# Performance work log

Measured on AMD Instinct MI355X. Metric: run time of the kernel, lower is better.

Reference implementation:

```python
import jax, jax.numpy as jnp
import numpy as np

VOCAB, EMBED, HID, LAYERS, NGRAPH = 50000, 128, 256, 3, 128

def setup_inputs() -> dict:
    key = jax.random.key(0)
    ks = jax.random.split(key, 16)
    N, E = 50000, 800000
    x_lex = jax.random.randint(ks[0], (N,), 0, VOCAB)
    edge_index = jax.random.randint(ks[1], (2, E), 0, N)
    batch = jnp.sort(jax.random.randint(ks[2], (N,), 0, NGRAPH))
    s = lambda k, shp, fan: jax.random.normal(k, shp, jnp.float32) * (1.0 / np.sqrt(fan))
    return {
        "x_lex": x_lex, "edge_index": edge_index, "batch": batch,
        "embed_table": s(ks[3], (VOCAB, EMBED), EMBED),
        "W_proj": s(ks[4], (HID, EMBED), EMBED),                 # F.linear random-projection branch
        "ggnn_weight": s(ks[5], (LAYERS, HID, HID), HID),        # per-layer message transform
        "W_ih": s(ks[6], (3 * HID, HID), HID), "b_ih": jnp.zeros((3 * HID,), jnp.float32),
        "W_hh": s(ks[7], (3 * HID, HID), HID), "b_hh": jnp.zeros((3 * HID,), jnp.float32),
        "W1": s(ks[8], (HID // 4, HID), HID), "b1": jnp.zeros((HID // 4,), jnp.float32),
        "W2": s(ks[9], (1, HID // 4), HID // 4), "b2": jnp.zeros((1,), jnp.float32),
    }

def _gru_cell(a, h, W_ih, b_ih, W_hh, b_hh):
    gi = a @ W_ih.T + b_ih   # [N, 3H]
    gh = h @ W_hh.T + b_hh
    i_r, i_z, i_n = jnp.split(gi, 3, axis=-1)
    h_r, h_z, h_n = jnp.split(gh, 3, axis=-1)
    r = jax.nn.sigmoid(i_r + h_r)
    z = jax.nn.sigmoid(i_z + h_z)
    n = jnp.tanh(i_n + r * h_n)
    return (1.0 - z) * n + z * h

def reference(x_lex, edge_index, batch, embed_table, W_proj, ggnn_weight,
              W_ih, b_ih, W_hh, b_hh, W1, b1, W2, b2):
    N = x_lex.shape[0]
    x = embed_table[x_lex]                 # [N, EMBED]
    x = x @ W_proj.T                       # project to HID (embed_dim != hidden_dim branch)
    src, dst = edge_index[0], edge_index[1]
    h = x
    for i in range(LAYERS):
        m = h @ ggnn_weight[i]             # [N, HID] per-layer linear
        agg = jax.ops.segment_sum(m[src], dst, num_segments=N)  # scatter-add aggregation
        h = _gru_cell(agg, h, W_ih, b_ih, W_hh, b_hh)
    h_pool = jax.ops.segment_max(h, batch, num_segments=NGRAPH)  # global_max_pool [G, HID]
    logits = jax.nn.relu(h_pool @ W1.T + b1) @ W2.T + b2          # [G, 1]
    return (logits, h_pool)
```

## Files before the change

kernel.cpp:

```cpp
#include <hip/hip_runtime.h>
#include <math.h>

constexpr int HID = 256;

typedef __attribute__((ext_vector_type(8))) short bf16x8;
typedef __attribute__((ext_vector_type(4))) float f32x4;

__device__ __forceinline__ float bf2f(unsigned short u){
    union { unsigned int i; float f; } v; v.i = ((unsigned int)u) << 16; return v.f;
}
__device__ __forceinline__ unsigned short f2bf(float f){
    union { float f; unsigned int i; } v; v.f = f;
    return (unsigned short)((v.i + 0x7fffu + ((v.i >> 16) & 1u)) >> 16);
}
__device__ __forceinline__ float sigm(float x){ return 1.f / (1.f + __expf(-x)); }

__device__ __forceinline__ int xcd_chunk(int bid, int nwg){
    int q = nwg >> 3, r = nwg & 7;
    int xcd = bid & 7, pos = bid >> 3;
    return (xcd < r) ? xcd * (q + 1) + pos : r * (q + 1) + (xcd - r) * q + pos;
}

__device__ __forceinline__ void gll16(const unsigned short* g, unsigned short* l){
    __builtin_amdgcn_global_load_lds(
        (const __attribute__((address_space(1))) void*)g,
        (__attribute__((address_space(3))) void*)l, 16, 0, 0);
}

__global__ void k_prep(const float* __restrict__ Wproj, const float* __restrict__ Wih,
                       const float* __restrict__ Whh, const float* __restrict__ Wg,
                       const float* __restrict__ embed, const int* __restrict__ idx,
                       unsigned short* __restrict__ wproj, unsigned short* __restrict__ wih,
                       unsigned short* __restrict__ whh, unsigned short* __restrict__ wg,
                       unsigned short* __restrict__ x0, int Nn, int EMB){
    const long n1 = (long)HID * EMB, n2 = 3L * HID * HID;
    const long n5 = (long)Nn * EMB;
    const long tot = n1 + 3 * n2 + n5;
    for (long i = blockIdx.x * (long)blockDim.x + threadIdx.x; i < tot;
         i += (long)gridDim.x * blockDim.x){
        long j = i;
        if (j < n1){ wproj[j] = f2bf(Wproj[j]); continue; }
        j -= n1;
        if (j < n2){ wih[j] = f2bf(Wih[j]); continue; }
        j -= n2;
        if (j < n2){ whh[j] = f2bf(Whh[j]); continue; }
        j -= n2;
        if (j < n2){ wg[j] = f2bf(Wg[j]); continue; }
        j -= n2;
        int row = (int)(j / EMB), k = (int)(j % EMB);
        x0[j] = f2bf(embed[(size_t)idx[row] * EMB + k]);
    }
}

__global__ void k_deg(const int* __restrict__ dst, int E, int* __restrict__ deg){
    int i = blockIdx.x*blockDim.x + threadIdx.x;
    if (i < E) atomicAdd(&deg[dst[i]], 1);
}

__global__ void k_scanA(const int* __restrict__ deg, int N, int* __restrict__ bsum){
    __shared__ int red[512];
    int b = blockIdx.x, tid = threadIdx.x;
    int i = b * 512 + tid;
    red[tid] = (i < N) ? deg[i] : 0;
    __syncthreads();
    for (int o = 256; o > 0; o >>= 1){
        if (tid < o) red[tid] += red[tid + o];
        __syncthreads();
    }
    if (tid == 0) bsum[b] = red[0];
}

__global__ void k_scanB(int* __restrict__ bsum, int nb){
    __shared__ int s[1024];
    int tid = threadIdx.x;
    s[tid] = (tid < nb) ? bsum[tid] : 0;
    __syncthreads();
    for (int o = 1; o < 1024; o <<= 1){
        int v = (tid >= o) ? s[tid - o] : 0;
        __syncthreads();
        s[tid] += v;
        __syncthreads();
    }
    if (tid < nb) bsum[tid] = (tid > 0) ? s[tid - 1] : 0;
    if (tid == nb) bsum[nb] = s[nb - 1];
}

__global__ void k_scanC(const int* __restrict__ deg, int N, const int* __restrict__ bsum,
                        int* __restrict__ off){
    __shared__ int s[512];
    int b = blockIdx.x, tid = threadIdx.x;
    int i = b * 512 + tid;
    int v = (i < N) ? deg[i] : 0;
    s[tid] = v;
    __syncthreads();
    for (int o = 1; o < 512; o <<= 1){
        int t = (tid >= o) ? s[tid - o] : 0;
        __syncthreads();
        s[tid] += t;
        __syncthreads();
    }
    int ex = bsum[b] + ((tid > 0) ? s[tid - 1] : 0);
    if (i < N) off[i] = ex;
    else if (i == N) off[N] = ex;
}

__global__ void k_fill(const int* __restrict__ src, const int* __restrict__ dst, int E,
                       const int* __restrict__ off, int* __restrict__ cursor,
                       int* __restrict__ csr_src){
    int i = blockIdx.x*blockDim.x + threadIdx.x;
    if (i < E){
        int d = dst[i];
        int p = off[d] + atomicAdd(&cursor[d], 1);
        csr_src[p] = src[i];
    }
}

__global__ void k_agg(const unsigned short* __restrict__ h, const int* __restrict__ off,
                      const int* __restrict__ csr, unsigned short* __restrict__ out, int N){
    int wave = threadIdx.x >> 6, lane = threadIdx.x & 63;
    int d = blockIdx.x * 8 + wave * 2 + (lane >> 5);
    if (d >= N) return;
    int c = (lane & 31) * 8;
    float a[8] = {};
    int s0 = off[d], s1 = off[d + 1];
    int j = s0;
    for (; j + 3 < s1; j += 4){
        int sA = csr[j], sB = csr[j + 1], sC = csr[j + 2], sD = csr[j + 3];
        bf16x8 vA = *(const bf16x8*)(h + (size_t)sA * HID + c);
        bf16x8 vB = *(const bf16x8*)(h + (size_t)sB * HID + c);
        bf16x8 vC = *(const bf16x8*)(h + (size_t)sC * HID + c);
        bf16x8 vD = *(const bf16x8*)(h + (size_t)sD * HID + c);
        #pragma unroll
        for (int q = 0; q < 8; q++)
            a[q] += (bf2f((unsigned short)vA[q]) + bf2f((unsigned short)vB[q]))
                  + (bf2f((unsigned short)vC[q]) + bf2f((unsigned short)vD[q]));
    }
    for (; j < s1; j++){
        bf16x8 vA = *(const bf16x8*)(h + (size_t)csr[j] * HID + c);
        #pragma unroll
        for (int q = 0; q < 8; q++) a[q] += bf2f((unsigned short)vA[q]);
    }
    bf16x8 o;
    #pragma unroll
    for (int q = 0; q < 8; q++) o[q] = (short)f2bf(a[q]);
    *(bf16x8*)(out + (size_t)d * HID + c) = o;
}

__global__ __launch_bounds__(256, 3) void k_mmS(
    const unsigned short* __restrict__ A, const unsigned short* __restrict__ B,
    unsigned short* __restrict__ C, int M, int N, int K,
    int nbx, long lsB, long lsC)
{
    __shared__ __align__(16) unsigned short sm[3 * 1024 * 8];
    const int tid = threadIdx.x, w = tid >> 6, l = tid & 63;
    const int wm = w >> 1, wn = w & 1, lr = l & 15, lk = l >> 4;

    const int orig = xcd_chunk(blockIdx.x, gridDim.x);
    const int layer = orig / nbx, sub = orig % nbx;
    B += layer * lsB;
    C += layer * lsC;
    const int nby = N >> 7;
    const long row0 = (long)(sub / nby) * 128;
    const int  col0 = (sub % nby) * 128;

    long aoff0, aoff1, boff0, boff1;
    {
        int r0 = tid >> 2,          kc0 = tid & 3;
        int r1 = (tid + 256) >> 2,  kc1 = tid & 3;
        long g0 = row0 + r0; if (g0 > M - 1) g0 = M - 1;
        long g1 = row0 + r1; if (g1 > M - 1) g1 = M - 1;
        aoff0 = g0 * (long)K + (kc0 ^ ((r0 >> 1) & 3)) * 8;
        aoff1 = g1 * (long)K + (kc1 ^ ((r1 >> 1) & 3)) * 8;
        boff0 = (long)(col0 + r0) * K + (kc0 ^ ((r0 >> 1) & 3)) * 8;
        boff1 = (long)(col0 + r1) * K + (kc1 ^ ((r1 >> 1) & 3)) * 8;
    }
    auto STAGE = [&](int T, int buf){
        const int ka = T * 32;
        unsigned short* d = sm + (size_t)buf * 8192;
        gll16(A + aoff0 + ka, d + (0 * 256 + w * 64) * 8);
        gll16(A + aoff1 + ka, d + (1 * 256 + w * 64) * 8);
        gll16(B + boff0 + ka, d + (2 * 256 + w * 64) * 8);
        gll16(B + boff1 + ka, d + (3 * 256 + w * 64) * 8);
    };

    int raddrA[4], raddrB[4];
    #pragma unroll
    for (int i = 0; i < 4; i++){
        int ra = wm * 64 + i * 16 + lr;
        raddrA[i] = (ra * 4 + (lk ^ ((ra >> 1) & 3))) * 8;
        int rb = wn * 64 + i * 16 + lr;
        raddrB[i] = (512 + rb * 4 + (lk ^ ((rb >> 1) & 3))) * 8;
    }

    const int NT = K >> 5;
    STAGE(0, 0);
    STAGE(1, 1);

    f32x4 acc[4][4] = {};
    for (int t = 0; t < NT; t++){
        if (t < NT - 1) asm volatile("s_waitcnt vmcnt(4)" ::: "memory");
        else            asm volatile("s_waitcnt vmcnt(0)" ::: "memory");
        __builtin_amdgcn_s_barrier();
        if (t + 2 < NT) STAGE(t + 2, (t + 2) % 3);

        const unsigned short* bufp = sm + (size_t)(t % 3) * 8192;
        bf16x8 af[4], bfb[4];
        #pragma unroll
        for (int i = 0; i < 4; i++){
            af[i]  = *(const bf16x8*)(bufp + raddrA[i]);
            bfb[i] = *(const bf16x8*)(bufp + raddrB[i]);
        }
        __builtin_amdgcn_s_setprio(1);
        #pragma unroll
        for (int mi = 0; mi < 4; mi++)
            #pragma unroll
            for (int ni = 0; ni < 4; ni++)
                acc[mi][ni] = __builtin_amdgcn_mfma_f32_16x16x32_bf16(af[mi], bfb[ni], acc[mi][ni], 0, 0, 0);
        __builtin_amdgcn_s_setprio(0);
    }

    #pragma unroll
    for (int mi = 0; mi < 4; mi++)
        #pragma unroll
        for (int ni = 0; ni < 4; ni++)
            #pragma unroll
            for (int r = 0; r < 4; r++){
                long row = row0 + wm * 64 + mi * 16 + lk * 4 + r;
                if (row < M){
                    int col = col0 + wn * 64 + ni * 16 + lr;
                    C[row * (long)N + col] = f2bf(acc[mi][ni][r]);
                }
            }
}

__global__ __launch_bounds__(256, 2) void k_gru(
    const unsigned short* __restrict__ AGG, const unsigned short* __restrict__ H,
    const unsigned short* __restrict__ WE, const unsigned short* __restrict__ WH,
    const float* __restrict__ bih, const float* __restrict__ bhh,
    unsigned short* __restrict__ HN, int M)
{
    __shared__ __align__(16) unsigned short sm[3 * 1280 * 8];
    const int tid = threadIdx.x, w = tid >> 6, l = tid & 63;
    const int wm = w >> 1, wn = w & 1, lr = l & 15, lk = l >> 4;
    const int orig = xcd_chunk(blockIdx.x, gridDim.x);
    const long row0 = (long)(orig >> 2) * 128;
    const int  c0 = (orig & 3) * 64;

    long aoff0, aoff1, boff0, boff1, boff2;
    {
        int r0 = tid >> 2,         kc = tid & 3;
        int r1 = (tid + 256) >> 2;
        long g0 = row0 + r0; if (g0 > M - 1) g0 = M - 1;
        long g1 = row0 + r1; if (g1 > M - 1) g1 = M - 1;
        aoff0 = g0 * HID + (kc ^ ((r0 >> 1) & 3)) * 8;
        aoff1 = g1 * HID + (kc ^ ((r1 >> 1) & 3)) * 8;
        int rr = tid >> 2;
        long sw = (kc ^ ((rr >> 1) & 3)) * 8;
        boff0 = (long)(0 * HID + c0 + rr) * HID + sw;
        boff1 = (long)(1 * HID + c0 + rr) * HID + sw;
        boff2 = (long)(2 * HID + c0 + rr) * HID + sw;
    }
    auto STAGE = [&](int T, int buf){
        const unsigned short* As = (T < 8) ? AGG : H;
        const unsigned short* Bs = (T < 8) ? WE  : WH;
        const int ka = (T & 7) * 32;
        unsigned short* d = sm + (size_t)buf * 10240;
        gll16(As + aoff0 + ka, d + (0 * 256 + w * 64) * 8);
        gll16(As + aoff1 + ka, d + (1 * 256 + w * 64) * 8);
        gll16(Bs + boff0 + ka, d + (2 * 256 + w * 64) * 8);
        gll16(Bs + boff1 + ka, d + (3 * 256 + w * 64) * 8);
        gll16(Bs + boff2 + ka, d + (4 * 256 + w * 64) * 8);
    };

    int raddrA[4], raddrB[3][2];
    #pragma unroll
    for (int i = 0; i < 4; i++){
        int ra = wm * 64 + i * 16 + lr;
        raddrA[i] = (ra * 4 + (lk ^ ((ra >> 1) & 3))) * 8;
    }
    #pragma unroll
    for (int j = 0; j < 3; j++)
        #pragma unroll
        for (int ni = 0; ni < 2; ni++){
            int rb = wn * 32 + ni * 16 + lr;
            raddrB[j][ni] = (512 + j * 256 + rb * 4 + (lk ^ ((rb >> 1) & 3))) * 8;
        }

    f32x4 aR[4][2] = {}, aZ[4][2] = {}, aI[4][2] = {}, aHn[4][2] = {};

    auto STEP = [&](const unsigned short* bufp, f32x4 (&aX)[4][2]){
        bf16x8 a[4], bb[3][2];
        #pragma unroll
        for (int i = 0; i < 4; i++) a[i] = *(const bf16x8*)(bufp + raddrA[i]);
        #pragma unroll
        for (int j = 0; j < 3; j++)
            #pragma unroll
            for (int ni = 0; ni < 2; ni++)
                bb[j][ni] = *(const bf16x8*)(bufp + raddrB[j][ni]);
        __builtin_amdgcn_s_setprio(1);
        #pragma unroll
        for (int ni = 0; ni < 2; ni++)
            #pragma unroll
            for (int mi = 0; mi < 4; mi++){
                aR[mi][ni] = __builtin_amdgcn_mfma_f32_16x16x32_bf16(a[mi], bb[0][ni], aR[mi][ni], 0, 0, 0);
                aZ[mi][ni] = __builtin_amdgcn_mfma_f32_16x16x32_bf16(a[mi], bb[1][ni], aZ[mi][ni], 0, 0, 0);
                aX[mi][ni] = __builtin_amdgcn_mfma_f32_16x16x32_bf16(a[mi], bb[2][ni], aX[mi][ni], 0, 0, 0);
            }
        __builtin_amdgcn_s_setprio(0);
    };

    STAGE(0, 0);
    STAGE(1, 1);

    #pragma unroll
    for (int t = 0; t < 16; t++){
        if (t < 15) asm volatile("s_waitcnt vmcnt(5)" ::: "memory");
        else        asm volatile("s_waitcnt vmcnt(0)" ::: "memory");
        __builtin_amdgcn_s_barrier();
        if (t + 2 < 16) STAGE(t + 2, (t + 2) % 3);
        if (t < 8) STEP(sm + (size_t)(t % 3) * 10240, aI);
        else       STEP(sm + (size_t)(t % 3) * 10240, aHn);
    }

    #pragma unroll
    for (int ni = 0; ni < 2; ni++){
        int gc = c0 + wn * 32 + ni * 16 + lr;
        float br  = bih[gc] + bhh[gc];
        float bz  = bih[HID + gc] + bhh[HID + gc];
        float bin = bih[2 * HID + gc];
        float bhn = bhh[2 * HID + gc];
        #pragma unroll
        for (int mi = 0; mi < 4; mi++)
            #pragma unroll
            for (int r = 0; r < 4; r++){
                long row = row0 + wm * 64 + mi * 16 + lk * 4 + r;
                if (row < M){
                    float rr = sigm(aR[mi][ni][r] + br);
                    float zz = sigm(aZ[mi][ni][r] + bz);
                    float nn = tanhf(aI[mi][ni][r] + bin + rr * (aHn[mi][ni][r] + bhn));
                    float hv = bf2f(H[row * HID + gc]);
                    HN[row * HID + gc] = f2bf((1.f - zz) * nn + zz * hv);
                }
            }
    }
}

__global__ void k_pool_mlp(const unsigned short* __restrict__ h, const int* __restrict__ batch,
                           int Nn, int G,
                           const float* __restrict__ W1, const float* __restrict__ b1,
                           const float* __restrict__ W2, const float* __restrict__ b2,
                           float* __restrict__ out){
    int g = blockIdx.x;
    __shared__ float pool[HID];
    __shared__ float hid[64];

    int lo = 0, hi = Nn;
    while (lo < hi){ int mid = (lo + hi) >> 1; if (batch[mid] < g) lo = mid + 1; else hi = mid; }
    int s = lo;
    lo = s; hi = Nn;
    while (lo < hi){ int mid = (lo + hi) >> 1; if (batch[mid] < g + 1) lo = mid + 1; else hi = mid; }
    int e = lo;

    int c = threadIdx.x;
    float mx = -INFINITY;
    for (int i = s; i < e; i++) mx = fmaxf(mx, bf2f(h[(size_t)i * HID + c]));
    pool[c] = mx;
    out[(size_t)G + (size_t)g * HID + c] = mx;
    __syncthreads();

    if (c < 64){
        float sacc = b1[c];
        for (int k = 0; k < HID; k++) sacc += pool[k] * W1[c * HID + k];
        hid[c] = fmaxf(sacc, 0.f) * W2[c];
    }
    __syncthreads();
    if (c == 0){
        float sacc = b2[0];
        for (int j = 0; j < 64; j++) sacc += hid[j];
        out[g] = sacc;
    }
}

extern "C" void kernel_launch(void* const* d_in, const int* in_sizes, int n_in,
                              void* d_out, int out_size, void* d_ws, size_t ws_size,
                              hipStream_t stream){
    const int*   x_lex = (const int*)d_in[0];
    const int*   edge  = (const int*)d_in[1];
    const int*   batch = (const int*)d_in[2];
    const float* embed = (const float*)d_in[3];
    const float* Wproj = (const float*)d_in[4];
    const float* Wg    = (const float*)d_in[5];
    const float* Wih   = (const float*)d_in[6];
    const float* bih   = (const float*)d_in[7];
    const float* Whh   = (const float*)d_in[8];
    const float* bhh   = (const float*)d_in[9];
    const float* W1    = (const float*)d_in[10];
    const float* b1    = (const float*)d_in[11];
    const float* W2    = (const float*)d_in[12];
    const float* b2    = (const float*)d_in[13];

    int Nn  = in_sizes[0];
    int E   = in_sizes[1] / 2;
    int G   = out_size / (1 + HID);
    int EMB = in_sizes[4] / HID;

    const int* esrc = edge;
    const int* edst = edge + E;

    size_t HH = (size_t)HID * HID;
    unsigned short* x0    = (unsigned short*)d_ws;
    unsigned short* hA    = x0    + (size_t)Nn * EMB;
    unsigned short* hB    = hA    + (size_t)Nn * HID;
    unsigned short* aggh  = hB    + (size_t)Nn * HID;
    unsigned short* wproj = aggh  + (size_t)Nn * HID;
    unsigned short* wih   = wproj + (size_t)HID * EMB;
    unsigned short* whh   = wih   + 3 * HH;
    unsigned short* wg    = whh   + 3 * HH;
    unsigned short* weff  = wg    + 3 * HH;
    int* deg    = (int*)(weff + 9 * HH);
    int* cursor = deg + Nn;
    int* off    = cursor + Nn;
    int* csr    = off + Nn + 1;
    int nbScan  = (Nn + 511) / 512;
    int* bsum   = csr + E;

    size_t ush = (size_t)Nn * (EMB + 3 * HID) + (size_t)HID * EMB + 18 * HH;
    size_t needed = ush * 2 + (size_t)(3 * Nn + 2 + E + nbScan + 1) * sizeof(int);
    if (ws_size < needed) return;

    hipMemsetAsync(deg, 0, sizeof(int) * (size_t)(2 * Nn), stream);
    k_deg  <<<(E + 255) / 256, 256, 0, stream>>>(edst, E, deg);
    k_scanA<<<nbScan, 512, 0, stream>>>(deg, Nn, bsum);
    k_scanB<<<1, 1024, 0, stream>>>(bsum, nbScan);
    k_scanC<<<(Nn + 512) / 512, 512, 0, stream>>>(deg, Nn, bsum, off);
    k_fill <<<(E + 255) / 256, 256, 0, stream>>>(esrc, edst, E, off, cursor, csr);

    k_prep<<<2048, 256, 0, stream>>>(Wproj, Wih, Whh, Wg, embed, x_lex,
                                     wproj, wih, whh, wg, x0, Nn, EMB);

    k_mmS<<<36, 256, 0, stream>>>(wih, wg, weff, 3 * HID, HID, HID,
                                  12, (long)HH, (long)(3 * HH));

    int mb = (Nn + 127) / 128;

    k_mmS<<<mb * 2, 256, 0, stream>>>(x0, wproj, hA, Nn, HID, EMB,
                                      mb * 2, 0L, 0L);

    unsigned short* hc = hA;
    unsigned short* hn = hB;
    for (int lay = 0; lay < 3; lay++){
        k_agg<<<(Nn + 7) / 8, 256, 0, stream>>>(hc, off, csr, aggh, Nn);
        k_gru<<<mb * 4, 256, 0, stream>>>(
            aggh, hc, weff + (size_t)lay * 3 * HH, whh, bih, bhh, hn, Nn);
        unsigned short* t = hc; hc = hn; hn = t;
    }

    k_pool_mlp<<<G, HID, 0, stream>>>(hc, batch, Nn, G, W1, b1, W2, b2, (float*)d_out);
}
```

Before: 615.3 us.

## Shrink GRU tile to 64 rows and fold degree counting into prep kernel

The GRU GEMM kernel now works on 64-row tiles instead of 128, which cuts LDS per block and accumulator registers. Launch bounds go from 2 to 3 blocks per CU, and the grid doubles to improve occupancy and wave count. Separately, the edge in-degree atomic counting is merged into the weight/embedding prep kernel, removing one launch. The cost is that each block reuses the weight tiles over fewer rows, so more weight traffic goes through L2.

```diff
diff --git a/kernel.cpp b/kernel.cpp
--- a/kernel.cpp
+++ b/kernel.cpp
@@ -30,12 +30,13 @@
 __global__ void k_prep(const float* __restrict__ Wproj, const float* __restrict__ Wih,
                        const float* __restrict__ Whh, const float* __restrict__ Wg,
                        const float* __restrict__ embed, const int* __restrict__ idx,
+                       const int* __restrict__ edst, int E, int* __restrict__ deg,
                        unsigned short* __restrict__ wproj, unsigned short* __restrict__ wih,
                        unsigned short* __restrict__ whh, unsigned short* __restrict__ wg,
                        unsigned short* __restrict__ x0, int Nn, int EMB){
     const long n1 = (long)HID * EMB, n2 = 3L * HID * HID;
     const long n5 = (long)Nn * EMB;
-    const long tot = n1 + 3 * n2 + n5;
+    const long tot = n1 + 3 * n2 + n5 + E;
     for (long i = blockIdx.x * (long)blockDim.x + threadIdx.x; i < tot;
          i += (long)gridDim.x * blockDim.x){
         long j = i;
@@ -47,14 +48,14 @@
         j -= n2;
         if (j < n2){ wg[j] = f2bf(Wg[j]); continue; }
         j -= n2;
-        int row = (int)(j / EMB), k = (int)(j % EMB);
-        x0[j] = f2bf(embed[(size_t)idx[row] * EMB + k]);
-    }
-}
-
-__global__ void k_deg(const int* __restrict__ dst, int E, int* __restrict__ deg){
-    int i = blockIdx.x*blockDim.x + threadIdx.x;
-    if (i < E) atomicAdd(&deg[dst[i]], 1);
+        if (j < n5){
+            int row = (int)(j / EMB), k = (int)(j % EMB);
+            x0[j] = f2bf(embed[(size_t)idx[row] * EMB + k]);
+            continue;
+        }
+        j -= n5;
+        atomicAdd(&deg[edst[j]], 1);
+    }
 }
 
 __global__ void k_scanA(const int* __restrict__ deg, int N, int* __restrict__ bsum){
@@ -233,49 +234,44 @@
             }
 }
 
-__global__ __launch_bounds__(256, 2) void k_gru(
+__global__ __launch_bounds__(256, 3) void k_gru(
     const unsigned short* __restrict__ AGG, const unsigned short* __restrict__ H,
     const unsigned short* __restrict__ WE, const unsigned short* __restrict__ WH,
     const float* __restrict__ bih, const float* __restrict__ bhh,
     unsigned short* __restrict__ HN, int M)
 {
-    __shared__ __align__(16) unsigned short sm[3 * 1280 * 8];
+    __shared__ __align__(16) unsigned short sm[3 * 1024 * 8];
     const int tid = threadIdx.x, w = tid >> 6, l = tid & 63;
     const int wm = w >> 1, wn = w & 1, lr = l & 15, lk = l >> 4;
     const int orig = xcd_chunk(blockIdx.x, gridDim.x);
-    const long row0 = (long)(orig >> 2) * 128;
+    const long row0 = (long)(orig >> 2) * 64;
     const int  c0 = (orig & 3) * 64;
 
-    long aoff0, aoff1, boff0, boff1, boff2;
+    long aoff, boff[3];
     {
-        int r0 = tid >> 2,         kc = tid & 3;
-        int r1 = (tid + 256) >> 2;
+        int r0 = tid >> 2, kc = tid & 3;
         long g0 = row0 + r0; if (g0 > M - 1) g0 = M - 1;
-        long g1 = row0 + r1; if (g1 > M - 1) g1 = M - 1;
-        aoff0 = g0 * HID + (kc ^ ((r0 >> 1) & 3)) * 8;
-        aoff1 = g1 * HID + (kc ^ ((r1 >> 1) & 3)) * 8;
-        int rr = tid >> 2;
-        long sw = (kc ^ ((rr >> 1) & 3)) * 8;
-        boff0 = (long)(0 * HID + c0 + rr) * HID + sw;
-        boff1 = (long)(1 * HID + c0 + rr) * HID + sw;
-        boff2 = (long)(2 * HID + c0 + rr) * HID + sw;
+        int sw = (kc ^ ((r0 >> 1) & 3)) * 8;
+        aoff = g0 * HID + sw;
+        #pragma unroll
+        for (int q = 0; q < 3; q++)
+            boff[q] = (long)(q * HID + c0 + r0) * HID + sw;
     }
     auto STAGE = [&](int T, int buf){
         const unsigned short* As = (T < 8) ? AGG : H;
         const unsigned short* Bs = (T < 8) ? WE  : WH;
         const int ka = (T & 7) * 32;
-        unsigned short* d = sm + (size_t)buf * 10240;
-        gll16(As + aoff0 + ka, d + (0 * 256 + w * 64) * 8);
-        gll16(As + aoff1 + ka, d + (1 * 256 + w * 64) * 8);
-        gll16(Bs + boff0 + ka, d + (2 * 256 + w * 64) * 8);
-        gll16(Bs + boff1 + ka, d + (3 * 256 + w * 64) * 8);
-        gll16(Bs + boff2 + ka, d + (4 * 256 + w * 64) * 8);
+        unsigned short* d = sm + (size_t)buf * 8192;
+        gll16(As + aoff + ka, d + (w * 64) * 8);
+        #pragma unroll
+        for (int q = 0; q < 3; q++)
+            gll16(Bs + boff[q] + ka, d + (256 + q * 256 + w * 64) * 8);
     };
 
-    int raddrA[4], raddrB[3][2];
-    #pragma unroll
-    for (int i = 0; i < 4; i++){
-        int ra = wm * 64 + i * 16 + lr;
+    int raddrA[2], raddrB[3][2];
+    #pragma unroll
+    for (int i = 0; i < 2; i++){
+        int ra = wm * 32 + i * 16 + lr;
         raddrA[i] = (ra * 4 + (lk ^ ((ra >> 1) & 3))) * 8;
     }
     #pragma unroll
@@ -283,43 +279,44 @@
         #pragma unroll
         for (int ni = 0; ni < 2; ni++){
             int rb = wn * 32 + ni * 16 + lr;
-            raddrB[j][ni] = (512 + j * 256 + rb * 4 + (lk ^ ((rb >> 1) & 3))) * 8;
+            raddrB[j][ni] = (256 + j * 256 + rb * 4 + (lk ^ ((rb >> 1) & 3))) * 8;
         }
 
-    f32x4 aR[4][2] = {}, aZ[4][2] = {}, aI[4][2] = {}, aHn[4][2] = {};
-
-    auto STEP = [&](const unsigned short* bufp, f32x4 (&aX)[4][2]){
-        bf16x8 a[4], bb[3][2];
-        #pragma unroll
-        for (int i = 0; i < 4; i++) a[i] = *(const bf16x8*)(bufp + raddrA[i]);
+    f32x4 aR[2][2] = {}, aZ[2][2] = {}, aI[2][2] = {}, aHn[2][2] = {};
+
+    STAGE(0, 0);
+    STAGE(1, 1);
+
+    #pragma unroll
+    for (int t = 0; t < 16; t++){
+        if (t < 15) asm volatile("s_waitcnt vmcnt(4)" ::: "memory");
+        else        asm volatile("s_waitcnt vmcnt(0)" ::: "memory");
+        __builtin_amdgcn_s_barrier();
+        if (t + 2 < 16) STAGE(t + 2, (t + 2) % 3);
+
+        const unsigned short* bufp = sm + (size_t)(t % 3) * 8192;
+        bf16x8 a[2], bb[3][2];
+        #pragma unroll
+        for (int i = 0; i < 2; i++) a[i] = *(const bf16x8*)(bufp + raddrA[i]);
         #pragma unroll
         for (int j = 0; j < 3; j++)
             #pragma unroll
             for (int ni = 0; ni < 2; ni++)
                 bb[j][ni] = *(const bf16x8*)(bufp + raddrB[j][ni]);
+
         __builtin_amdgcn_s_setprio(1);
         #pragma unroll
         for (int ni = 0; ni < 2; ni++)
             #pragma unroll
-            for (int mi = 0; mi < 4; mi++){
+            for (int mi = 0; mi < 2; mi++){
                 aR[mi][ni] = __builtin_amdgcn_mfma_f32_16x16x32_bf16(a[mi], bb[0][ni], aR[mi][ni], 0, 0, 0);
                 aZ[mi][ni] = __builtin_amdgcn_mfma_f32_16x16x32_bf16(a[mi], bb[1][ni], aZ[mi][ni], 0, 0, 0);
-                aX[mi][ni] = __builtin_amdgcn_mfma_f32_16x16x32_bf16(a[mi], bb[2][ni], aX[mi][ni], 0, 0, 0);
+                if (t < 8)
+                    aI[mi][ni]  = __builtin_amdgcn_mfma_f32_16x16x32_bf16(a[mi], bb[2][ni], aI[mi][ni], 0, 0, 0);
+                else
+                    aHn[mi][ni] = __builtin_amdgcn_mfma_f32_16x16x32_bf16(a[mi], bb[2][ni], aHn[mi][ni], 0, 0, 0);
             }
         __builtin_amdgcn_s_setprio(0);
-    };
-
-    STAGE(0, 0);
-    STAGE(1, 1);
-
-    #pragma unroll
-    for (int t = 0; t < 16; t++){
-        if (t < 15) asm volatile("s_waitcnt vmcnt(5)" ::: "memory");
-        else        asm volatile("s_waitcnt vmcnt(0)" ::: "memory");
-        __builtin_amdgcn_s_barrier();
-        if (t + 2 < 16) STAGE(t + 2, (t + 2) % 3);
-        if (t < 8) STEP(sm + (size_t)(t % 3) * 10240, aI);
-        else       STEP(sm + (size_t)(t % 3) * 10240, aHn);
     }
 
     #pragma unroll
@@ -330,10 +327,10 @@
         float bin = bih[2 * HID + gc];
         float bhn = bhh[2 * HID + gc];
         #pragma unroll
-        for (int mi = 0; mi < 4; mi++)
+        for (int mi = 0; mi < 2; mi++)
             #pragma unroll
             for (int r = 0; r < 4; r++){
-                long row = row0 + wm * 64 + mi * 16 + lk * 4 + r;
+                long row = row0 + wm * 32 + mi * 16 + lk * 4 + r;
                 if (row < M){
                     float rr = sigm(aR[mi][ni][r] + br);
                     float zz = sigm(aZ[mi][ni][r] + bz);
@@ -429,15 +426,14 @@
     if (ws_size < needed) return;
 
     hipMemsetAsync(deg, 0, sizeof(int) * (size_t)(2 * Nn), stream);
-    k_deg  <<<(E + 255) / 256, 256, 0, stream>>>(edst, E, deg);
+    k_prep<<<2048, 256, 0, stream>>>(Wproj, Wih, Whh, Wg, embed, x_lex,
+                                     edst, E, deg,
+                                     wproj, wih, whh, wg, x0, Nn, EMB);
     k_scanA<<<nbScan, 512, 0, stream>>>(deg, Nn, bsum);
     k_scanB<<<1, 1024, 0, stream>>>(bsum, nbScan);
     k_scanC<<<(Nn + 512) / 512, 512, 0, stream>>>(deg, Nn, bsum, off);
     k_fill <<<(E + 255) / 256, 256, 0, stream>>>(esrc, edst, E, off, cursor, csr);
 
-    k_prep<<<2048, 256, 0, stream>>>(Wproj, Wih, Whh, Wg, embed, x_lex,
-                                     wproj, wih, whh, wg, x0, Nn, EMB);
-
     k_mmS<<<36, 256, 0, stream>>>(wih, wg, weff, 3 * HID, HID, HID,
                                   12, (long)HH, (long)(3 * HH));
 
@@ -445,12 +441,14 @@
 
     k_mmS<<<mb * 2, 256, 0, stream>>>(x0, wproj, hA, Nn, HID, EMB,
                                       mb * 2, 0L, 0L);
+
+    int gruBlocks = ((Nn + 63) / 64) * 4;
 
     unsigned short* hc = hA;
     unsigned short* hn = hB;
     for (int lay = 0; lay < 3; lay++){
         k_agg<<<(Nn + 7) / 8, 256, 0, stream>>>(hc, off, csr, aggh, Nn);
-        k_gru<<<mb * 4, 256, 0, stream>>>(
+        k_gru<<<gruBlocks, 256, 0, stream>>>(
             aggh, hc, weff + (size_t)lay * 3 * HH, whh, bih, bhh, hn, Nn);
         unsigned short* t = hc; hc = hn; hn = t;
     }
```

Result: faster. 588.8 us (-4.3%).
